# Performance work log

Measured on AMD Instinct MI355X. Metric: run time of the kernel, lower is better.

## Reference

```python
import jax, jax.numpy as jnp
import numpy as np

S = 4096          # seq_len (longformer-large-4096)
H = 1024          # hidden_size
FF = 3072         # ffnn_size (hardcoded)
G = 100           # number of gold mentions
MAX_SPAN = 30     # max_span_length
TOP_LAMBDA = 0.2
LN_EPS = 1e-5
MASK_VAL = 10000.0


def setup_inputs() -> dict:
    key = jax.random.key(0)
    ks = jax.random.split(key, 16)
    sc = 0.02
    sequence_output = jax.random.normal(ks[0], (1, S, H), jnp.float32)
    attention_mask = jnp.ones((1, S), jnp.int32)
    # valid gold spans: 1 <= start <= end < start + MAX_SPAN (so torch's >0 filter keeps all)
    gs = jax.random.randint(ks[1], (G,), 1, S - MAX_SPAN)
    gl = jax.random.randint(ks[2], (G,), 0, MAX_SPAN)
    gold_mentions = jnp.stack([gs, gs + gl], axis=1).astype(jnp.int32)  # [G, 2]
    inp = {
        'sequence_output': sequence_output,
        'attention_mask': attention_mask,
        'gold_mentions': gold_mentions,
        # start_mention_mlp
        'W_sm': jax.random.normal(ks[3], (H, FF), jnp.float32) * sc,
        'b_sm': jnp.zeros((FF,), jnp.float32),
        'g_sm': jnp.ones((FF,), jnp.float32),
        'beta_sm': jnp.zeros((FF,), jnp.float32),
        # end_mention_mlp
        'W_em': jax.random.normal(ks[4], (H, FF), jnp.float32) * sc,
        'b_em': jnp.zeros((FF,), jnp.float32),
        'g_em': jnp.ones((FF,), jnp.float32),
        'beta_em': jnp.zeros((FF,), jnp.float32),
        # classifiers
        'w_start': jax.random.normal(ks[5], (FF,), jnp.float32) * sc,
        'b_start': jnp.zeros((), jnp.float32),
        'w_end': jax.random.normal(ks[6], (FF,), jnp.float32) * sc,
        'b_end': jnp.zeros((), jnp.float32),
        'W_s2e': jax.random.normal(ks[7], (FF, FF), jnp.float32) * sc,
        'b_s2e': jnp.zeros((FF,), jnp.float32),
    }
    return inp


def _fcl(x, W, b, g, beta):
    # dense -> gelu (exact) -> layernorm (dropout is identity in eval)
    h = jax.nn.gelu(x @ W + b, approximate=False)
    mu = jnp.mean(h, axis=-1, keepdims=True)
    var = jnp.mean(jnp.square(h - mu), axis=-1, keepdims=True)
    return (h - mu) * jax.lax.rsqrt(var + LN_EPS) * g + beta


def _forward(sequence_output, attention_mask, gold_mentions,
             W_sm, b_sm, g_sm, beta_sm, W_em, b_em, g_em, beta_em,
             w_start, b_start, w_end, b_end, W_s2e, b_s2e):
    start_reps = _fcl(sequence_output, W_sm, b_sm, g_sm, beta_sm)  # [1,S,FF]
    end_reps = _fcl(sequence_output, W_em, b_em, g_em, beta_em)    # [1,S,FF]

    start_logits = jnp.einsum('bsf,f->bs', start_reps, w_start) + b_start  # [1,S]
    end_logits = jnp.einsum('bsf,f->bs', end_reps, w_end) + b_end          # [1,S]
    temp = start_reps @ W_s2e + b_s2e                                      # [1,S,FF]
    joint = jnp.einsum('bsf,btf->bst', temp, end_reps)                     # [1,S,S]
    mention_logits = joint + start_logits[:, :, None] + end_logits[:, None, :]

    # span mask: start <= end < start + MAX_SPAN (triu(0) then tril(MAX_SPAN-1))
    i = jnp.arange(S)
    mention_mask = ((i[:, None] <= i[None, :]) & (i[None, :] < i[:, None] + MAX_SPAN)
                    ).astype(jnp.float32)[None]  # [1,S,S]
    mention_logits = jnp.clip(mention_logits + (1.0 - mention_mask) * (-MASK_VAL),
                              -MASK_VAL, MASK_VAL)

    # top-k pruning; attention_mask is full so k is static: int(S * 0.2)
    max_k = int(S * TOP_LAMBDA)  # 819
    _, topk_1d = jax.lax.top_k(mention_logits.reshape(1, -1), max_k)  # [1,max_k]
    sorted_idx = jnp.sort(topk_1d, axis=-1)
    topk_start_ids = sorted_idx // S
    topk_end_ids = sorted_idx % S
    span_mask = jnp.ones((1, max_k), jnp.float32)

    # losses
    probs = jax.nn.sigmoid(mention_logits)  # [1,S,S]
    gstart = gold_mentions[:, 0]
    gend = gold_mentions[:, 1]
    gold_probs = probs[0, gstart, gend]
    # torch BCE clamps log at -100
    cost_gold = -jnp.mean(jnp.maximum(jnp.log(gold_probs), -100.0))
    junk = probs.at[0, gstart, gend].set(0.0)
    log1mp = jnp.maximum(jnp.log(1.0 - junk), -100.0)
    cost_junk = -jnp.sum(jnp.where(mention_mask == 1.0, log1mp, 0.0)) / jnp.sum(mention_mask)
    cost_is_mention = (cost_gold + cost_junk)[None]  # [1]

    return topk_start_ids, topk_end_ids, span_mask, sequence_output, cost_is_mention


def reference(sequence_output, attention_mask, gold_mentions,
              W_sm, b_sm, g_sm, beta_sm, W_em, b_em, g_em, beta_em,
              w_start, b_start, w_end, b_end, W_s2e, b_s2e):
    return _forward(sequence_output, attention_mask, gold_mentions,
                    W_sm, b_sm, g_sm, beta_sm, W_em, b_em, g_em, beta_em,
                    w_start, b_start, w_end, b_end, W_s2e, b_s2e)
```

## Files before the change

### kernel.cpp

```cpp
#include <hip/hip_runtime.h>
#include <math.h>

#define S 4096
#define H 1024
#define FF 3072
#define G 100
#define MAXSPAN 30
#define MAXK 819
#define NBAND (S * MAXSPAN)
#define BAND_COUNT 122445.0

#define O_START 0
#define O_END   819
#define O_MASK  1638
#define O_SEQ   2457
#define O_COST  (2457 + S * H)

typedef __bf16 bf16x8 __attribute__((ext_vector_type(8)));
typedef float f32x16 __attribute__((ext_vector_type(16)));


__device__ __forceinline__ float block_reduce_256(float x, volatile float* red) {
  #pragma unroll
  for (int off = 32; off > 0; off >>= 1) x += __shfl_down(x, off, 64);
  int wid = threadIdx.x >> 6;
  int lane = threadIdx.x & 63;
  __syncthreads();
  if (lane == 0) red[wid] = x;
  __syncthreads();
  return red[0] + red[1] + red[2] + red[3];
}

__device__ __forceinline__ float block_reduce_1024(float x, volatile float* red) {
  #pragma unroll
  for (int off = 32; off > 0; off >>= 1) x += __shfl_down(x, off, 64);
  int wid = threadIdx.x >> 6;
  int lane = threadIdx.x & 63;
  __syncthreads();
  if (lane == 0) red[wid] = x;
  __syncthreads();
  float s = 0.f;
  #pragma unroll
  for (int q = 0; q < 16; q++) s += red[q];
  return s;
}

__device__ __forceinline__ unsigned f2key(float f) {
  unsigned b = __float_as_uint(f);
  return (b & 0x80000000u) ? ~b : (b | 0x80000000u);
}

__device__ __forceinline__ unsigned short bf16_rne(float x) {
  unsigned u = __float_as_uint(x);
  unsigned r = ((u >> 16) & 1u) + 0x7FFFu;
  return (unsigned short)((u + r) >> 16);
}

__device__ __forceinline__ void split2(float x, unsigned short& h, unsigned short& l) {
  h = bf16_rne(x);
  float hf = __uint_as_float(((unsigned)h) << 16);
  l = bf16_rne(x - hf);
}

__device__ __forceinline__ void gld16(const void* g, void* l) {
  __builtin_amdgcn_global_load_lds(
      (const __attribute__((address_space(1))) unsigned int*)g,
      (__attribute__((address_space(3))) unsigned int*)l, 16, 0, 0);
}


__global__ __launch_bounds__(256) void pack_a_kernel(const float* __restrict__ A,
                                                     unsigned short* __restrict__ hi,
                                                     unsigned short* __restrict__ lo,
                                                     int K) {
  __shared__ float tile[32][33];
  const int t = threadIdx.x;
  const int tx = t & 31, ty8 = t >> 5;
  const int k0 = blockIdx.x * 32, r0 = blockIdx.y * 32;
  #pragma unroll
  for (int r = ty8; r < 32; r += 8)
    tile[r][tx] = A[(size_t)(r0 + r) * K + k0 + tx];
  __syncthreads();
  if (t < 128) {
    const int kql = t >> 5;
    const int rl = t & 31;
    unsigned short h8[8], l8[8];
    #pragma unroll
    for (int s = 0; s < 8; s++) split2(tile[rl][kql * 8 + s], h8[s], l8[s]);
    const size_t panel = (size_t)(r0 >> 7);
    const int rloc = (r0 & 127) + rl;
    const size_t off = panel * (size_t)(128 * K) + (size_t)(k0 / 8 + kql) * 1024 + (size_t)rloc * 8;
    *(uint4*)(hi + off) = *(const uint4*)h8;
    *(uint4*)(lo + off) = *(const uint4*)l8;
  }
}

__global__ __launch_bounds__(256) void pack_ln_a_kernel(const float* __restrict__ A,
                                                        const float* __restrict__ mu,
                                                        const float* __restrict__ rstd,
                                                        const float* __restrict__ g,
                                                        const float* __restrict__ beta,
                                                        unsigned short* __restrict__ hi,
                                                        unsigned short* __restrict__ lo,
                                                        int K) {
  __shared__ float tile[32][33];
  const int t = threadIdx.x;
  const int tx = t & 31, ty8 = t >> 5;
  const int k0 = blockIdx.x * 32, r0 = blockIdx.y * 32;
  #pragma unroll
  for (int r = ty8; r < 32; r += 8)
    tile[r][tx] = A[(size_t)(r0 + r) * K + k0 + tx];
  __syncthreads();
  if (t < 128) {
    const int kql = t >> 5;
    const int rl = t & 31;
    const int row = r0 + rl;
    const float m = mu[row], rs = rstd[row];
    float4 g0 = *(const float4*)(g + k0 + kql * 8);
    float4 g1 = *(const float4*)(g + k0 + kql * 8 + 4);
    float4 b0 = *(const float4*)(beta + k0 + kql * 8);
    float4 b1 = *(const float4*)(beta + k0 + kql * 8 + 4);
    float gv[8] = {g0.x, g0.y, g0.z, g0.w, g1.x, g1.y, g1.z, g1.w};
    float bv[8] = {b0.x, b0.y, b0.z, b0.w, b1.x, b1.y, b1.z, b1.w};
    unsigned short h8[8], l8[8];
    #pragma unroll
    for (int s = 0; s < 8; s++) {
      float v = (tile[rl][kql * 8 + s] - m) * rs * gv[s] + bv[s];
      split2(v, h8[s], l8[s]);
    }
    const size_t panel = (size_t)(r0 >> 7);
    const int rloc = (r0 & 127) + rl;
    const size_t off = panel * (size_t)(128 * K) + (size_t)(k0 / 8 + kql) * 1024 + (size_t)rloc * 8;
    *(uint4*)(hi + off) = *(const uint4*)h8;
    *(uint4*)(lo + off) = *(const uint4*)l8;
  }
}

__device__ __forceinline__ void pack_bt_body(const float* __restrict__ W,
                                             unsigned short* __restrict__ hi,
                                             unsigned short* __restrict__ lo,
                                             int K, int N) {
  __shared__ float tile[32][33];
  const int t = threadIdx.x;
  const int tx = t & 31, ty8 = t >> 5;
  const int k0 = blockIdx.x * 32, n0 = blockIdx.y * 32;
  #pragma unroll
  for (int r = ty8; r < 32; r += 8)
    tile[r][tx] = W[(size_t)(k0 + r) * N + n0 + tx];
  __syncthreads();
  if (t < 128) {
    const int kql = t >> 5;
    const int nl = t & 31;
    unsigned short h8[8], l8[8];
    #pragma unroll
    for (int s = 0; s < 8; s++) split2(tile[kql * 8 + s][nl], h8[s], l8[s]);
    const size_t panel = (size_t)(n0 >> 7);
    const int nloc = (n0 & 127) + nl;
    const size_t off = panel * (size_t)(128 * K) + (size_t)(k0 / 8 + kql) * 1024 + (size_t)nloc * 8;
    *(uint4*)(hi + off) = *(const uint4*)h8;
    *(uint4*)(lo + off) = *(const uint4*)l8;
  }
}

__global__ __launch_bounds__(256) void pack_bt_kernel(const float* __restrict__ W,
                                                      unsigned short* __restrict__ hi,
                                                      unsigned short* __restrict__ lo,
                                                      int K, int N) {
  pack_bt_body(W, hi, lo, K, N);
}

__global__ __launch_bounds__(256) void pack_bt_dual_kernel(const float* __restrict__ W1,
                                                           const float* __restrict__ W2,
                                                           unsigned short* __restrict__ h1,
                                                           unsigned short* __restrict__ l1,
                                                           unsigned short* __restrict__ h2,
                                                           unsigned short* __restrict__ l2,
                                                           int K, int N) {
  if (blockIdx.z == 0) pack_bt_body(W1, h1, l1, K, N);
  else                 pack_bt_body(W2, h2, l2, K, N);
}


template <int EPI>
__device__ __forceinline__ void gemm_body(const char* cAh, const char* cAl,
                                          const char* cBh, const char* cBl,
                                          const float* __restrict__ bias,
                                          float* __restrict__ C,
                                          int bm, int bn, int N, int K,
                                          char* smem) {
  const int tid = threadIdx.x;
  const int lane = tid & 63;
  const int wid = __builtin_amdgcn_readfirstlane(tid >> 6);
  const int wm = wid >> 1, wn = wid & 1;
  const int lb = lane * 16;
  const int ldsq = wid * 2048;

  const int khalf = lane >> 5;
  const int r31 = lane & 31;
  const int abase = khalf * 2048 + (wm * 64 + r31) * 16;
  const int bbase = khalf * 2048 + (wn * 64 + r31) * 16;

  f32x16 acc[2][2];
  #pragma unroll
  for (int a = 0; a < 2; a++)
    #pragma unroll
    for (int b = 0; b < 2; b++)
      #pragma unroll
      for (int r = 0; r < 16; r++) acc[a][b][r] = 0.0f;

  auto stage = [&](int buf, int k0) {
    const size_t qb = (size_t)((k0 >> 3) + wid) * 2048 + lb;
    char* sbuf = smem + buf * 32768 + ldsq;
    gld16(cAh + qb,        sbuf +     0);
    gld16(cAh + qb + 1024, sbuf +     0 + 1024);
    gld16(cAl + qb,        sbuf +  8192);
    gld16(cAl + qb + 1024, sbuf +  8192 + 1024);
    gld16(cBh + qb,        sbuf + 16384);
    gld16(cBh + qb + 1024, sbuf + 16384 + 1024);
    gld16(cBl + qb,        sbuf + 24576);
    gld16(cBl + qb + 1024, sbuf + 24576 + 1024);
  };

  stage(0, 0);
  for (int k0 = 0; k0 < K; k0 += 32) {
    const int cur = (k0 >> 5) & 1;
    __syncthreads();
    if (k0 + 32 < K) stage(cur ^ 1, k0 + 32);
    const char* sm = smem + cur * 32768;

    bf16x8 ah[2][2], al[2][2], bh[2][2], bl[2][2];
    #pragma unroll
    for (int ks = 0; ks < 2; ks++) {
      #pragma unroll
      for (int mt = 0; mt < 2; mt++) {
        ah[ks][mt] = *(const bf16x8*)(sm +     0 + ks * 4096 + abase + mt * 512);
        al[ks][mt] = *(const bf16x8*)(sm +  8192 + ks * 4096 + abase + mt * 512);
      }
      #pragma unroll
      for (int nt = 0; nt < 2; nt++) {
        bh[ks][nt] = *(const bf16x8*)(sm + 16384 + ks * 4096 + bbase + nt * 512);
        bl[ks][nt] = *(const bf16x8*)(sm + 24576 + ks * 4096 + bbase + nt * 512);
      }
    }
    #pragma unroll
    for (int ks = 0; ks < 2; ks++)
      #pragma unroll
      for (int mt = 0; mt < 2; mt++)
        #pragma unroll
        for (int nt = 0; nt < 2; nt++) {
          acc[mt][nt] = __builtin_amdgcn_mfma_f32_32x32x16_bf16(ah[ks][mt], bh[ks][nt], acc[mt][nt], 0, 0, 0);
          acc[mt][nt] = __builtin_amdgcn_mfma_f32_32x32x16_bf16(al[ks][mt], bh[ks][nt], acc[mt][nt], 0, 0, 0);
          acc[mt][nt] = __builtin_amdgcn_mfma_f32_32x32x16_bf16(ah[ks][mt], bl[ks][nt], acc[mt][nt], 0, 0, 0);
        }
  }

  #pragma unroll
  for (int mt = 0; mt < 2; mt++) {
    #pragma unroll
    for (int nt = 0; nt < 2; nt++) {
      const int colg = bn + wn * 64 + nt * 32 + r31;
      const float bb = bias[colg];
      #pragma unroll
      for (int reg = 0; reg < 16; reg++) {
        const int rowl = (reg & 3) + 8 * (reg >> 2) + 4 * khalf;
        const int rowg = bm + wm * 64 + mt * 32 + rowl;
        float v = acc[mt][nt][reg] + bb;
        if (EPI == 1) v = 0.5f * v * (1.0f + erff(v * 0.70710678118654752f));
        C[(size_t)rowg * N + colg] = v;
      }
    }
  }
}

__global__ __launch_bounds__(256) void gemm_mfma_kernel(const unsigned short* __restrict__ Ahi,
                                                        const unsigned short* __restrict__ Alo,
                                                        const unsigned short* __restrict__ Bhi,
                                                        const unsigned short* __restrict__ Blo,
                                                        const float* __restrict__ bias,
                                                        float* __restrict__ C,
                                                        int N, int K) {
  __shared__ __align__(16) char smem[65536];
  const size_t panAb = (size_t)blockIdx.y * (size_t)(128 * K) * 2;
  const size_t panBb = (size_t)blockIdx.x * (size_t)(128 * K) * 2;
  gemm_body<0>((const char*)Ahi + panAb, (const char*)Alo + panAb,
               (const char*)Bhi + panBb, (const char*)Blo + panBb,
               bias, C, blockIdx.y * 128, blockIdx.x * 128, N, K, smem);
}

__global__ __launch_bounds__(256) void gemm_mfma_dual_kernel(const unsigned short* __restrict__ Ahi,
                                                             const unsigned short* __restrict__ Alo,
                                                             const unsigned short* __restrict__ B1hi,
                                                             const unsigned short* __restrict__ B1lo,
                                                             const unsigned short* __restrict__ B2hi,
                                                             const unsigned short* __restrict__ B2lo,
                                                             const float* __restrict__ bias1,
                                                             const float* __restrict__ bias2,
                                                             float* __restrict__ C1,
                                                             float* __restrict__ C2,
                                                             int N, int K) {
  __shared__ __align__(16) char smem[65536];
  const int zb = blockIdx.z;
  const unsigned short* Bhi = zb ? B2hi : B1hi;
  const unsigned short* Blo = zb ? B2lo : B1lo;
  const float* bias = zb ? bias2 : bias1;
  float* C = zb ? C2 : C1;
  const size_t panAb = (size_t)blockIdx.y * (size_t)(128 * K) * 2;
  const size_t panBb = (size_t)blockIdx.x * (size_t)(128 * K) * 2;
  gemm_body<1>((const char*)Ahi + panAb, (const char*)Alo + panAb,
               (const char*)Bhi + panBb, (const char*)Blo + panBb,
               bias, C, blockIdx.y * 128, blockIdx.x * 128, N, K, smem);
}


__global__ __launch_bounds__(256) void ln_stats_kernel(const float* __restrict__ HbS,
                                                       const float* __restrict__ HbE,
                                                       const float* __restrict__ gS,
                                                       const float* __restrict__ betaS,
                                                       const float* __restrict__ wS,
                                                       const float* __restrict__ bS,
                                                       const float* __restrict__ gE,
                                                       const float* __restrict__ betaE,
                                                       const float* __restrict__ wE,
                                                       const float* __restrict__ bE,
                                                       float* __restrict__ slog,
                                                       float* __restrict__ elog,
                                                       float* __restrict__ muS,
                                                       float* __restrict__ rstdS,
                                                       float* __restrict__ muE,
                                                       float* __restrict__ rstdE) {
  __shared__ float red[4];
  const int row = blockIdx.x, tid = threadIdx.x;
  const int br = blockIdx.y;
  const float* Hb = br ? HbE : HbS;
  const float* g = br ? gE : gS;
  const float* beta = br ? betaE : betaS;
  const float* w = br ? wE : wS;
  const float* bsc = br ? bE : bS;
  const float* h = Hb + (size_t)row * FF;

  float4 v[3];
  float s = 0.0f;
  #pragma unroll
  for (int t = 0; t < 3; t++) {
    v[t] = *(const float4*)(h + tid * 4 + t * 1024);
    s += v[t].x + v[t].y + v[t].z + v[t].w;
  }
  float mu = block_reduce_256(s, red) * (1.0f / (float)FF);

  float s2 = 0.0f;
  #pragma unroll
  for (int t = 0; t < 3; t++) {
    float dx = v[t].x - mu, dy = v[t].y - mu, dz = v[t].z - mu, dw = v[t].w - mu;
    s2 += dx * dx + dy * dy + dz * dz + dw * dw;
  }
  float var = block_reduce_256(s2, red) * (1.0f / (float)FF);
  float rstd = rsqrtf(var + 1e-5f);

  float dot = 0.0f;
  #pragma unroll
  for (int t = 0; t < 3; t++) {
    int idx = tid * 4 + t * 1024;
    float4 gv = *(const float4*)(g + idx);
    float4 bv = *(const float4*)(beta + idx);
    float4 wv = *(const float4*)(w + idx);
    float rx = (v[t].x - mu) * rstd * gv.x + bv.x;
    float ry = (v[t].y - mu) * rstd * gv.y + bv.y;
    float rz = (v[t].z - mu) * rstd * gv.z + bv.z;
    float rw = (v[t].w - mu) * rstd * gv.w + bv.w;
    dot += rx * wv.x + ry * wv.y + rz * wv.z + rw * wv.w;
  }
  float dt = block_reduce_256(dot, red);
  if (tid == 0) {
    if (br) { elog[row] = dt + bsc[0]; muE[row] = mu; rstdE[row] = rstd; }
    else    { slog[row] = dt + bsc[0]; muS[row] = mu; rstdS[row] = rstd; }
  }
}


__global__ __launch_bounds__(256) void band_joint_kernel(const float* __restrict__ T,
                                                         const float* __restrict__ Eraw,
                                                         const float* __restrict__ muE,
                                                         const float* __restrict__ rstdE,
                                                         const float* __restrict__ gE,
                                                         const float* __restrict__ betaE,
                                                         const float* __restrict__ sl,
                                                         const float* __restrict__ el,
                                                         float* __restrict__ band,
                                                         double* __restrict__ jacc) {
  __shared__ float Elds[45][260];
  __shared__ float red[4];
  const int t = threadIdx.x;
  const int bx = blockIdx.x;
  const int sbx = (bx & 7) * 32 + (bx >> 3);
  const int i0 = sbx * 16;
  const int r_l = t >> 4, c = t & 15;

  float accd[MAXSPAN];
  #pragma unroll
  for (int d = 0; d < MAXSPAN; d++) accd[d] = 0.0f;

  for (int k0 = 0; k0 < FF; k0 += 256) {
    const float* trow = T + (size_t)(i0 + r_l) * FF + k0 + c * 16;
    float4 tv0 = *(const float4*)(trow + 0);
    float4 tv1 = *(const float4*)(trow + 4);
    float4 tv2 = *(const float4*)(trow + 8);
    float4 tv3 = *(const float4*)(trow + 12);
    __syncthreads();
    for (int rr = t >> 6; rr < 45; rr += 4) {
      int gr = i0 + rr;
      int cc = (t & 63) * 4;
      float4 rv = {0.f, 0.f, 0.f, 0.f};
      if (gr < S) {
        float4 ev = *(const float4*)(Eraw + (size_t)gr * FF + k0 + cc);
        float m = muE[gr], rs = rstdE[gr];
        float4 gv = *(const float4*)(gE + k0 + cc);
        float4 bv = *(const float4*)(betaE + k0 + cc);
        rv.x = (ev.x - m) * rs * gv.x + bv.x;
        rv.y = (ev.y - m) * rs * gv.y + bv.y;
        rv.z = (ev.z - m) * rs * gv.z + bv.z;
        rv.w = (ev.w - m) * rs * gv.w + bv.w;
      }
      *(float4*)&Elds[rr][cc] = rv;
    }
    __syncthreads();
    #pragma unroll
    for (int d = 0; d < MAXSPAN; d++) {
      const float* er = &Elds[r_l + d][c * 16];
      float4 e0 = *(const float4*)(er + 0);
      float4 e1 = *(const float4*)(er + 4);
      float4 e2 = *(const float4*)(er + 8);
      float4 e3 = *(const float4*)(er + 12);
      accd[d] += tv0.x * e0.x + tv0.y * e0.y + tv0.z * e0.z + tv0.w * e0.w
               + tv1.x * e1.x + tv1.y * e1.y + tv1.z * e1.z + tv1.w * e1.w
               + tv2.x * e2.x + tv2.y * e2.y + tv2.z * e2.z + tv2.w * e2.w
               + tv3.x * e3.x + tv3.y * e3.y + tv3.z * e3.z + tv3.w * e3.w;
    }
  }

  const int i = i0 + r_l;
  const float my_sl = sl[i];
  float jsum = 0.0f;
  #pragma unroll
  for (int d = 0; d < MAXSPAN; d++) {
    float v = accd[d];
    v += __shfl_down(v, 8, 16);
    v += __shfl_down(v, 4, 16);
    v += __shfl_down(v, 2, 16);
    v += __shfl_down(v, 1, 16);
    if (c == 0) {
      int j = i + d;
      if (j < S) {
        float vv = v + my_sl + el[j];
        vv = fminf(fmaxf(vv, -10000.0f), 10000.0f);
        band[i * MAXSPAN + d] = vv;
        float p = 1.0f / (1.0f + expf(-vv));
        jsum += fmaxf(logf(1.0f - p), -100.0f);
      } else {
        band[i * MAXSPAN + d] = -1e30f;
      }
    }
  }
  float tot = block_reduce_256(jsum, red);
  if (t == 0) atomicAdd(jacc, (double)tot);
}


__global__ __launch_bounds__(1024) void topk_finalize_kernel(const float* __restrict__ band,
                                                             const int* __restrict__ gold,
                                                             const double* __restrict__ jacc,
                                                             float* __restrict__ out) {
  __shared__ int hist[256];
  __shared__ unsigned sh_prefix;
  __shared__ int sh_remk;
  __shared__ int idxbuf[1024];
  __shared__ unsigned tkey[256];
  __shared__ int tidx[256];
  __shared__ int cnt_gt, cnt_eq;
  __shared__ int sb[1024];
  __shared__ int gcell[G];
  __shared__ float redf[16];
  const int tid = threadIdx.x;

  if (tid < 256) hist[tid] = 0;
  __syncthreads();
  for (int e = tid; e < NBAND; e += 1024)
    atomicAdd(&hist[f2key(band[e]) >> 24], 1);
  __syncthreads();
  if (tid == 0) {
    int cum = 0, b = 255;
    for (; b > 0; b--) {
      if (cum + hist[b] >= MAXK) break;
      cum += hist[b];
    }
    sh_prefix = (unsigned)b;
    sh_remk = MAXK - cum;
  }
  __syncthreads();
  const unsigned p8 = sh_prefix;
  int remk = sh_remk;
  __syncthreads();

  if (tid < 256) hist[tid] = 0;
  __syncthreads();
  for (int e = tid; e < NBAND; e += 1024) {
    unsigned key = f2key(band[e]);
    if ((key >> 24) == p8) atomicAdd(&hist[(key >> 16) & 255], 1);
  }
  __syncthreads();
  if (tid == 0) {
    int cum = 0, b = 255;
    for (; b > 0; b--) {
      if (cum + hist[b] >= remk) break;
      cum += hist[b];
    }
    sh_prefix = (p8 << 8) | (unsigned)b;
    sh_remk = remk - cum;
  }
  __syncthreads();
  const unsigned T16 = sh_prefix;
  remk = sh_remk;

  if (tid == 0) { cnt_gt = 0; cnt_eq = 0; }
  __syncthreads();
  for (int e = tid; e < NBAND; e += 1024) {
    unsigned key = f2key(band[e]);
    unsigned k16 = key >> 16;
    if (k16 >= T16) {
      int i = e / MAXSPAN, d = e - i * MAXSPAN;
      int fi = i * S + i + d;
      if (k16 > T16) {
        int p = atomicAdd(&cnt_gt, 1);
        if (p < 1024) idxbuf[p] = fi;
      } else {
        int p = atomicAdd(&cnt_eq, 1);
        if (p < 256) { tkey[p] = key; tidx[p] = fi; }
      }
    }
  }
  __syncthreads();
  if (tid == 0) {
    int ngt = cnt_gt < 1024 ? cnt_gt : 1024;
    int ne = cnt_eq < 256 ? cnt_eq : 256;
    for (int a2 = 1; a2 < ne; a2++) {
      unsigned kv = tkey[a2]; int iv = tidx[a2];
      int b2 = a2 - 1;
      while (b2 >= 0 && (tkey[b2] < kv || (tkey[b2] == kv && tidx[b2] > iv))) {
        tkey[b2 + 1] = tkey[b2]; tidx[b2 + 1] = tidx[b2]; b2--;
      }
      tkey[b2 + 1] = kv; tidx[b2 + 1] = iv;
    }
    int take = remk < ne ? remk : ne;
    for (int q = 0; q < take; q++)
      if (ngt + q < 1024) idxbuf[ngt + q] = tidx[q];
  }
  __syncthreads();

  sb[tid] = (tid < MAXK) ? idxbuf[tid] : 0x7FFFFFFF;
  __syncthreads();
  for (int ksz = 2; ksz <= 1024; ksz <<= 1) {
    for (int jj = ksz >> 1; jj > 0; jj >>= 1) {
      int ixj = tid ^ jj;
      if (ixj > tid) {
        int a2 = sb[tid], b2 = sb[ixj];
        bool up = ((tid & ksz) == 0);
        if (up ? (a2 > b2) : (a2 < b2)) { sb[tid] = b2; sb[ixj] = a2; }
      }
      __syncthreads();
    }
  }
  if (tid < MAXK) {
    int fi = sb[tid];
    out[O_START + tid] = (float)(fi >> 12);
    out[O_END + tid]   = (float)(fi & 4095);
    out[O_MASK + tid]  = 1.0f;
  }

  if (tid < G) {
    int gs = gold[2 * tid], ge = gold[2 * tid + 1];
    gcell[tid] = gs * MAXSPAN + (ge - gs);
  }
  __syncthreads();
  float tg = 0.0f, tj = 0.0f;
  if (tid < G) {
    int cell = gcell[tid];
    float x = band[cell];
    float p = 1.0f / (1.0f + expf(-x));
    tg = fmaxf(logf(p), -100.0f);
    bool first = true;
    for (int q = 0; q < tid; q++)
      if (gcell[q] == cell) { first = false; break; }
    if (first) tj = fmaxf(logf(1.0f - p), -100.0f);
  }
  float sg = block_reduce_1024(tg, redf);
  float sj = block_reduce_1024(tj, redf);
  if (tid == 0) {
    double junk = *jacc - (double)sj;
    double cost = -((double)sg / (double)G) - (junk / BAND_COUNT);
    out[O_COST] = (float)cost;
  }
}


extern "C" void kernel_launch(void* const* d_in, const int* in_sizes, int n_in,
                              void* d_out, int out_size, void* d_ws, size_t ws_size,
                              hipStream_t stream) {
  (void)in_sizes; (void)n_in; (void)out_size; (void)ws_size;
  const float* seq    = (const float*)d_in[0];
  const int*   gold   = (const int*)d_in[2];
  const float* W_sm   = (const float*)d_in[3];
  const float* b_sm   = (const float*)d_in[4];
  const float* g_sm   = (const float*)d_in[5];
  const float* be_sm  = (const float*)d_in[6];
  const float* W_em   = (const float*)d_in[7];
  const float* b_em   = (const float*)d_in[8];
  const float* g_em   = (const float*)d_in[9];
  const float* be_em  = (const float*)d_in[10];
  const float* w_st   = (const float*)d_in[11];
  const float* b_st   = (const float*)d_in[12];
  const float* w_en   = (const float*)d_in[13];
  const float* b_en   = (const float*)d_in[14];
  const float* W_s2e  = (const float*)d_in[15];
  const float* b_s2e  = (const float*)d_in[16];
  float* out = (float*)d_out;
  char* ws = (char*)d_ws;

  const size_t SZ_REP = (size_t)S * FF * 4;
  float*  bufS = (float*)(ws);
  float*  bufE = (float*)(ws + SZ_REP);
  float*  bufT = (float*)(ws + 2 * SZ_REP);
  char* R3 = ws + 3 * SZ_REP;
  unsigned short* seqhi = (unsigned short*)R3;
  unsigned short* seqlo = (unsigned short*)(R3 + (size_t)S * H * 2);
  unsigned short* a3hi  = (unsigned short*)R3;
  unsigned short* a3lo  = (unsigned short*)(R3 + (size_t)S * FF * 2);
  char* R4 = ws + 4 * SZ_REP;
  const size_t SZ_W12 = (size_t)H * FF * 2;
  unsigned short* wb1hi = (unsigned short*)R4;
  unsigned short* wb1lo = (unsigned short*)(R4 + SZ_W12);
  unsigned short* wb2hi = (unsigned short*)(R4 + 2 * SZ_W12);
  unsigned short* wb2lo = (unsigned short*)(R4 + 3 * SZ_W12);
  unsigned short* wbhi = (unsigned short*)R4;
  unsigned short* wblo = (unsigned short*)(R4 + (size_t)FF * FF * 2);
  char* R5 = R4 + 2 * (size_t)FF * FF * 2;
  float*  band = (float*)R5;
  double* jacc = (double*)(R5 + (size_t)NBAND * 4);
  float*  slog = (float*)(R5 + (size_t)NBAND * 4 + 64);
  float*  elog  = slog + S;
  float*  muS   = elog + S;
  float*  rstdS = muS + S;
  float*  muE   = rstdS + S;
  float*  rstdE = muE + S;

  hipMemsetAsync(jacc, 0, 8, stream);

  dim3 gg(FF / 128, S / 128);
  dim3 gg2(FF / 128, S / 128, 2);

  pack_a_kernel<<<dim3(H / 32, S / 32), 256, 0, stream>>>(seq, seqhi, seqlo, H);
  pack_bt_dual_kernel<<<dim3(H / 32, FF / 32, 2), 256, 0, stream>>>(W_sm, W_em,
                                                                    wb1hi, wb1lo, wb2hi, wb2lo, H, FF);
  gemm_mfma_dual_kernel<<<gg2, 256, 0, stream>>>(seqhi, seqlo, wb1hi, wb1lo, wb2hi, wb2lo,
                                                 b_sm, b_em, bufS, bufE, FF, H);
  ln_stats_kernel<<<dim3(S, 2), 256, 0, stream>>>(bufS, bufE, g_sm, be_sm, w_st, b_st,
                                                  g_em, be_em, w_en, b_en,
                                                  slog, elog, muS, rstdS, muE, rstdE);
  pack_ln_a_kernel<<<dim3(FF / 32, S / 32), 256, 0, stream>>>(bufS, muS, rstdS, g_sm, be_sm, a3hi, a3lo, FF);
  pack_bt_kernel<<<dim3(FF / 32, FF / 32), 256, 0, stream>>>(W_s2e, wbhi, wblo, FF, FF);
  gemm_mfma_kernel<<<gg, 256, 0, stream>>>(a3hi, a3lo, wbhi, wblo, b_s2e, bufT, FF, FF);

  band_joint_kernel<<<S / 16, 256, 0, stream>>>(bufT, bufE, muE, rstdE, g_em, be_em,
                                                slog, elog, band, jacc);

  topk_finalize_kernel<<<1, 1024, 0, stream>>>(band, gold, jacc, out);

  hipMemcpyAsync(out + O_SEQ, seq, (size_t)S * H * 4, hipMemcpyDeviceToDevice, stream);
}
```

Baseline: 824.2 us.

## Fuse pack kernels, build top-k histogram in band kernel, fold seq copy

Merges the seq and weight pack launches into one grid, and the LN-A and W_s2e packs into another. The sequence_output passthrough copy is folded into the seq pack pass, removing a separate device-to-device memcpy. A 16-bit key histogram is now built with global atomics inside the band kernel, so the single-block top-k no longer makes two histogram passes over the band; it only does a prefix scan over the 64K bins. The cost is heavy global atomic contention on the histogram, plus a larger memset.

```diff
diff --git a/kernel.cpp b/kernel.cpp
--- a/kernel.cpp
+++ b/kernel.cpp
@@ -69,17 +69,21 @@
 }
 
 
-__global__ __launch_bounds__(256) void pack_a_kernel(const float* __restrict__ A,
-                                                     unsigned short* __restrict__ hi,
-                                                     unsigned short* __restrict__ lo,
-                                                     int K) {
+__device__ __forceinline__ void pack_a_body(const float* __restrict__ A,
+                                            float* __restrict__ Aout,
+                                            unsigned short* __restrict__ hi,
+                                            unsigned short* __restrict__ lo,
+                                            int K, int bx, int by) {
   __shared__ float tile[32][33];
   const int t = threadIdx.x;
   const int tx = t & 31, ty8 = t >> 5;
-  const int k0 = blockIdx.x * 32, r0 = blockIdx.y * 32;
-  #pragma unroll
-  for (int r = ty8; r < 32; r += 8)
-    tile[r][tx] = A[(size_t)(r0 + r) * K + k0 + tx];
+  const int k0 = bx * 32, r0 = by * 32;
+  #pragma unroll
+  for (int r = ty8; r < 32; r += 8) {
+    float v = A[(size_t)(r0 + r) * K + k0 + tx];
+    tile[r][tx] = v;
+    if (Aout) Aout[(size_t)(r0 + r) * K + k0 + tx] = v;
+  }
   __syncthreads();
   if (t < 128) {
     const int kql = t >> 5;
@@ -95,18 +99,18 @@
   }
 }
 
-__global__ __launch_bounds__(256) void pack_ln_a_kernel(const float* __restrict__ A,
-                                                        const float* __restrict__ mu,
-                                                        const float* __restrict__ rstd,
-                                                        const float* __restrict__ g,
-                                                        const float* __restrict__ beta,
-                                                        unsigned short* __restrict__ hi,
-                                                        unsigned short* __restrict__ lo,
-                                                        int K) {
+__device__ __forceinline__ void pack_ln_a_body(const float* __restrict__ A,
+                                               const float* __restrict__ mu,
+                                               const float* __restrict__ rstd,
+                                               const float* __restrict__ g,
+                                               const float* __restrict__ beta,
+                                               unsigned short* __restrict__ hi,
+                                               unsigned short* __restrict__ lo,
+                                               int K, int bx, int by) {
   __shared__ float tile[32][33];
   const int t = threadIdx.x;
   const int tx = t & 31, ty8 = t >> 5;
-  const int k0 = blockIdx.x * 32, r0 = blockIdx.y * 32;
+  const int k0 = bx * 32, r0 = by * 32;
   #pragma unroll
   for (int r = ty8; r < 32; r += 8)
     tile[r][tx] = A[(size_t)(r0 + r) * K + k0 + tx];
@@ -139,11 +143,11 @@
 __device__ __forceinline__ void pack_bt_body(const float* __restrict__ W,
                                              unsigned short* __restrict__ hi,
                                              unsigned short* __restrict__ lo,
-                                             int K, int N) {
+                                             int K, int N, int bx, int by) {
   __shared__ float tile[32][33];
   const int t = threadIdx.x;
   const int tx = t & 31, ty8 = t >> 5;
-  const int k0 = blockIdx.x * 32, n0 = blockIdx.y * 32;
+  const int k0 = bx * 32, n0 = by * 32;
   #pragma unroll
   for (int r = ty8; r < 32; r += 8)
     tile[r][tx] = W[(size_t)(k0 + r) * N + n0 + tx];
@@ -162,22 +166,35 @@
   }
 }
 
-__global__ __launch_bounds__(256) void pack_bt_kernel(const float* __restrict__ W,
-                                                      unsigned short* __restrict__ hi,
-                                                      unsigned short* __restrict__ lo,
-                                                      int K, int N) {
-  pack_bt_body(W, hi, lo, K, N);
-}
-
-__global__ __launch_bounds__(256) void pack_bt_dual_kernel(const float* __restrict__ W1,
-                                                           const float* __restrict__ W2,
-                                                           unsigned short* __restrict__ h1,
-                                                           unsigned short* __restrict__ l1,
-                                                           unsigned short* __restrict__ h2,
-                                                           unsigned short* __restrict__ l2,
-                                                           int K, int N) {
-  if (blockIdx.z == 0) pack_bt_body(W1, h1, l1, K, N);
-  else                 pack_bt_body(W2, h2, l2, K, N);
+__global__ __launch_bounds__(256) void pack_head_kernel(const float* __restrict__ seq,
+                                                        float* __restrict__ seq_out,
+                                                        unsigned short* __restrict__ sh,
+                                                        unsigned short* __restrict__ sl,
+                                                        const float* __restrict__ W1,
+                                                        const float* __restrict__ W2,
+                                                        unsigned short* __restrict__ w1h,
+                                                        unsigned short* __restrict__ w1l,
+                                                        unsigned short* __restrict__ w2h,
+                                                        unsigned short* __restrict__ w2l) {
+  const int y = blockIdx.y;
+  if (y < 128)      pack_a_body(seq, seq_out, sh, sl, H, blockIdx.x, y);
+  else if (y < 224) pack_bt_body(W1, w1h, w1l, H, FF, blockIdx.x, y - 128);
+  else              pack_bt_body(W2, w2h, w2l, H, FF, blockIdx.x, y - 224);
+}
+
+__global__ __launch_bounds__(256) void pack_mid_kernel(const float* __restrict__ bufS,
+                                                       const float* __restrict__ muS,
+                                                       const float* __restrict__ rstdS,
+                                                       const float* __restrict__ g,
+                                                       const float* __restrict__ beta,
+                                                       unsigned short* __restrict__ ahi,
+                                                       unsigned short* __restrict__ alo,
+                                                       const float* __restrict__ Ws2e,
+                                                       unsigned short* __restrict__ wbh,
+                                                       unsigned short* __restrict__ wbl) {
+  const int y = blockIdx.y;
+  if (y < 128) pack_ln_a_body(bufS, muS, rstdS, g, beta, ahi, alo, FF, blockIdx.x, y);
+  else         pack_bt_body(Ws2e, wbh, wbl, FF, FF, blockIdx.x, y - 128);
 }
 
 
@@ -386,7 +403,8 @@
                                                          const float* __restrict__ sl,
                                                          const float* __restrict__ el,
                                                          float* __restrict__ band,
-                                                         double* __restrict__ jacc) {
+                                                         double* __restrict__ jacc,
+                                                         unsigned* __restrict__ hist16) {
   __shared__ float Elds[45][260];
   __shared__ float red[4];
   const int t = threadIdx.x;
@@ -453,6 +471,7 @@
         float vv = v + my_sl + el[j];
         vv = fminf(fmaxf(vv, -10000.0f), 10000.0f);
         band[i * MAXSPAN + d] = vv;
+        atomicAdd(&hist16[f2key(vv) >> 16], 1u);
         float p = 1.0f / (1.0f + expf(-vv));
         jsum += fmaxf(logf(1.0f - p), -100.0f);
       } else {
@@ -468,10 +487,12 @@
 __global__ __launch_bounds__(1024) void topk_finalize_kernel(const float* __restrict__ band,
                                                              const int* __restrict__ gold,
                                                              const double* __restrict__ jacc,
+                                                             const unsigned* __restrict__ hist16,
                                                              float* __restrict__ out) {
-  __shared__ int hist[256];
-  __shared__ unsigned sh_prefix;
+  __shared__ int csum[1024];
+  __shared__ unsigned sh_T16;
   __shared__ int sh_remk;
+  __shared__ int sh_chunk, sh_above;
   __shared__ int idxbuf[1024];
   __shared__ unsigned tkey[256];
   __shared__ int tidx[256];
@@ -481,44 +502,34 @@
   __shared__ float redf[16];
   const int tid = threadIdx.x;
 
-  if (tid < 256) hist[tid] = 0;
-  __syncthreads();
-  for (int e = tid; e < NBAND; e += 1024)
-    atomicAdd(&hist[f2key(band[e]) >> 24], 1);
+  int s = 0;
+  #pragma unroll 8
+  for (int q = 0; q < 64; q++) s += (int)hist16[tid * 64 + q];
+  csum[tid] = s;
+  __syncthreads();
+  for (int off = 1; off < 1024; off <<= 1) {
+    int v = (tid + off < 1024) ? csum[tid + off] : 0;
+    __syncthreads();
+    csum[tid] += v;
+    __syncthreads();
+  }
+  {
+    int nxt = (tid < 1023) ? csum[tid + 1] : 0;
+    if (csum[tid] >= MAXK && nxt < MAXK) { sh_chunk = tid; sh_above = nxt; }
+  }
   __syncthreads();
   if (tid == 0) {
-    int cum = 0, b = 255;
-    for (; b > 0; b--) {
-      if (cum + hist[b] >= MAXK) break;
-      cum += hist[b];
-    }
-    sh_prefix = (unsigned)b;
-    sh_remk = MAXK - cum;
-  }
-  __syncthreads();
-  const unsigned p8 = sh_prefix;
+    int cum = sh_above;
+    int b = sh_chunk * 64 + 63;
+    for (;; b--) {
+      int h = (int)hist16[b];
+      if (cum + h >= MAXK || b == sh_chunk * 64) { sh_T16 = (unsigned)b; sh_remk = MAXK - cum; break; }
+      cum += h;
+    }
+  }
+  __syncthreads();
+  const unsigned T16 = sh_T16;
   int remk = sh_remk;
-  __syncthreads();
-
-  if (tid < 256) hist[tid] = 0;
-  __syncthreads();
-  for (int e = tid; e < NBAND; e += 1024) {
-    unsigned key = f2key(band[e]);
-    if ((key >> 24) == p8) atomicAdd(&hist[(key >> 16) & 255], 1);
-  }
-  __syncthreads();
-  if (tid == 0) {
-    int cum = 0, b = 255;
-    for (; b > 0; b--) {
-      if (cum + hist[b] >= remk) break;
-      cum += hist[b];
-    }
-    sh_prefix = (p8 << 8) | (unsigned)b;
-    sh_remk = remk - cum;
-  }
-  __syncthreads();
-  const unsigned T16 = sh_prefix;
-  remk = sh_remk;
 
   if (tid == 0) { cnt_gt = 0; cnt_eq = 0; }
   __syncthreads();
@@ -642,36 +653,34 @@
   unsigned short* wbhi = (unsigned short*)R4;
   unsigned short* wblo = (unsigned short*)(R4 + (size_t)FF * FF * 2);
   char* R5 = R4 + 2 * (size_t)FF * FF * 2;
-  float*  band = (float*)R5;
-  double* jacc = (double*)(R5 + (size_t)NBAND * 4);
-  float*  slog = (float*)(R5 + (size_t)NBAND * 4 + 64);
+  float*    band   = (float*)R5;
+  unsigned* hist16 = (unsigned*)(R5 + (size_t)NBAND * 4);
+  double*   jacc   = (double*)(R5 + (size_t)NBAND * 4 + 262144);
+  float*    slog   = (float*)(R5 + (size_t)NBAND * 4 + 262144 + 64);
   float*  elog  = slog + S;
   float*  muS   = elog + S;
   float*  rstdS = muS + S;
   float*  muE   = rstdS + S;
   float*  rstdE = muE + S;
 
-  hipMemsetAsync(jacc, 0, 8, stream);
+  hipMemsetAsync(hist16, 0, 262144 + 64 + 8, stream);
 
   dim3 gg(FF / 128, S / 128);
   dim3 gg2(FF / 128, S / 128, 2);
 
-  pack_a_kernel<<<dim3(H / 32, S / 32), 256, 0, stream>>>(seq, seqhi, seqlo, H);
-  pack_bt_dual_kernel<<<dim3(H / 32, FF / 32, 2), 256, 0, stream>>>(W_sm, W_em,
-                                                                    wb1hi, wb1lo, wb2hi, wb2lo, H, FF);
+  pack_head_kernel<<<dim3(32, 320), 256, 0, stream>>>(seq, out + O_SEQ, seqhi, seqlo,
+                                                      W_sm, W_em, wb1hi, wb1lo, wb2hi, wb2lo);
   gemm_mfma_dual_kernel<<<gg2, 256, 0, stream>>>(seqhi, seqlo, wb1hi, wb1lo, wb2hi, wb2lo,
                                                  b_sm, b_em, bufS, bufE, FF, H);
   ln_stats_kernel<<<dim3(S, 2), 256, 0, stream>>>(bufS, bufE, g_sm, be_sm, w_st, b_st,
                                                   g_em, be_em, w_en, b_en,
                                                   slog, elog, muS, rstdS, muE, rstdE);
-  pack_ln_a_kernel<<<dim3(FF / 32, S / 32), 256, 0, stream>>>(bufS, muS, rstdS, g_sm, be_sm, a3hi, a3lo, FF);
-  pack_bt_kernel<<<dim3(FF / 32, FF / 32), 256, 0, stream>>>(W_s2e, wbhi, wblo, FF, FF);
+  pack_mid_kernel<<<dim3(96, 224), 256, 0, stream>>>(bufS, muS, rstdS, g_sm, be_sm,
+                                                     a3hi, a3lo, W_s2e, wbhi, wblo);
   gemm_mfma_kernel<<<gg, 256, 0, stream>>>(a3hi, a3lo, wbhi, wblo, b_s2e, bufT, FF, FF);
 
   band_joint_kernel<<<S / 16, 256, 0, stream>>>(bufT, bufE, muE, rstdE, g_em, be_em,
-                                                slog, elog, band, jacc);
-
-  topk_finalize_kernel<<<1, 1024, 0, stream>>>(band, gold, jacc, out);
-
-  hipMemcpyAsync(out + O_SEQ, seq, (size_t)S * H * 4, hipMemcpyDeviceToDevice, stream);
-}
+                                                slog, elog, band, jacc, hist16);
+
+  topk_finalize_kernel<<<1, 1024, 0, stream>>>(band, gold, jacc, hist16, out);
+}
```

Result: faster. 796.2 us (-3.4%).
